# Kernel tuning notes

Hardware: AMD Instinct MI355X
Metric: run time of the kernel (lower is better)

The kernel has to match this reference:

```python
import jax, jax.numpy as jnp
import numpy as np

N = 100000          # nodes
E = 1600000         # edges
DIMS = [128, 64, 64, 47]  # in_feats -> hidden -> hidden -> n_classes
EPS = 1e-5


def setup_inputs() -> dict:
    key = jax.random.key(0)
    ks = jax.random.split(key, 10)
    d = {
        "features": jax.random.normal(ks[0], (N, DIMS[0]), jnp.float32),
        "src": jax.random.randint(ks[1], (E,), 0, N, dtype=jnp.int64),
        "dst": jax.random.randint(ks[2], (E,), 0, N, dtype=jnp.int64),
    }
    # GraphConv weights (glorot-ish) + bias
    for i in range(3):
        fan_in, fan_out = DIMS[i], DIMS[i + 1]
        scale = jnp.sqrt(2.0 / (fan_in + fan_out)).astype(jnp.float32)
        d[f"W{i}"] = jax.random.normal(ks[3 + i], (fan_in, fan_out), jnp.float32) * scale
        d[f"b{i}"] = jnp.zeros((fan_out,), jnp.float32)
    # BatchNorm affine params for the first two layers
    for i in range(2):
        d[f"gamma{i}"] = jnp.ones((DIMS[i + 1],), jnp.float32)
        d[f"beta{i}"] = jnp.zeros((DIMS[i + 1],), jnp.float32)
    return d


def _degree_isqrt(idx):
    # clamp degree to >=1 like DGL, then D^{-1/2}
    deg = jax.ops.segment_sum(jnp.ones((E,), jnp.float32), idx, num_segments=N)
    return jax.lax.rsqrt(jnp.maximum(deg, 1.0))


def _graph_conv(h, W, b, src, dst, out_isqrt, in_isqrt):
    # DGL GraphConv, norm='both': h' = D_in^{-1/2} A D_out^{-1/2} h W + b
    h = h * out_isqrt[:, None]
    if W.shape[0] > W.shape[1]:  # mult W first when it shrinks features (DGL order)
        h = h @ W
        h = jax.ops.segment_sum(h[src], dst, num_segments=N)
    else:
        h = jax.ops.segment_sum(h[src], dst, num_segments=N)
        h = h @ W
    return h * in_isqrt[:, None] + b


def _batch_norm(h, gamma, beta):
    mu = h.mean(axis=0)
    var = h.var(axis=0)  # biased, as torch BatchNorm uses for normalization
    return gamma * (h - mu) * jax.lax.rsqrt(var + EPS) + beta


def reference(features, src, dst, W0, b0, W1, b1, W2, b2,
              gamma0, beta0, gamma1, beta1):
    out_isqrt = _degree_isqrt(src)
    in_isqrt = _degree_isqrt(dst)
    Ws = [(W0, b0), (W1, b1), (W2, b2)]
    bns = [(gamma0, beta0), (gamma1, beta1)]
    h = features
    for i, (W, b) in enumerate(Ws):
        # dropout (p=0.5) before last layer only -> identity in eval mode
        h = _graph_conv(h, W, b, src, dst, out_isqrt, in_isqrt)
        if i < len(Ws) - 1:
            h = _batch_norm(h, *bns[i])
            h = jax.nn.relu(h)
    return h
```

## Files before the change

kernel.cpp:

```cpp
#include <hip/hip_runtime.h>
#include <hip/hip_bf16.h>
#include <hip/hip_fp16.h>

#define BN_EPS 1e-5f
#define N_MAX 100000
#define CAP 64
#define NB_MAX 391
#define BCAP 8192

typedef __attribute__((ext_vector_type(8))) _Float16 half8;
typedef __attribute__((ext_vector_type(4))) float floatx4;

__device__ __attribute__((aligned(16))) float g_wsf[130 * N_MAX + 16384];
__device__ int   g_wsi[(1 + CAP) * N_MAX + NB_MAX * BCAP + 2 * NB_MAX + 64];
__device__ unsigned char g_wsb[NB_MAX * BCAP];

__global__ __launch_bounds__(256)
void k_bin(const int* __restrict__ src, const int* __restrict__ dst,
           int* __restrict__ gcur, int* __restrict__ scur,
           int* __restrict__ pairs, unsigned char* __restrict__ sbytes,
           int E, int nb) {
    __shared__ int dh[NB_MAX], db[NB_MAX], dc[NB_MAX];
    __shared__ int sh[NB_MAX], sb[NB_MAX], sc[NB_MAX];
    const int tid = threadIdx.x;
    for (int i = tid; i < nb; i += 256) { dh[i] = 0; sh[i] = 0; dc[i] = 0; sc[i] = 0; }
    __syncthreads();
    const int e0 = blockIdx.x * 4096;
    int ss[16], dd[16];
#pragma unroll
    for (int i = 0; i < 16; ++i) {
        int e = e0 + i * 256 + tid;
        if (e < E) {
            ss[i] = src[e]; dd[i] = dst[e];
            atomicAdd(&dh[dd[i] >> 8], 1);
            atomicAdd(&sh[ss[i] >> 8], 1);
        } else ss[i] = -1;
    }
    __syncthreads();
    for (int i = tid; i < nb; i += 256) {
        db[i] = atomicAdd(&gcur[i], dh[i]);
        sb[i] = atomicAdd(&scur[i], sh[i]);
    }
    __syncthreads();
#pragma unroll
    for (int i = 0; i < 16; ++i) {
        if (ss[i] >= 0) {
            int b = dd[i] >> 8;
            int idx = db[b] + atomicAdd(&dc[b], 1);
            if (idx < BCAP) pairs[b * BCAP + idx] = (ss[i] << 8) | (dd[i] & 255);
            int b2 = ss[i] >> 8;
            int i2 = sb[b2] + atomicAdd(&sc[b2], 1);
            if (i2 < BCAP) sbytes[b2 * BCAP + i2] = (unsigned char)(ss[i] & 255);
        }
    }
}

__global__ __launch_bounds__(256)
void k_slab(const int* __restrict__ gcur, const int* __restrict__ pairs,
            int* __restrict__ slab, int* __restrict__ cnt,
            float* __restrict__ isq_d, int n) {
    __shared__ int c[256];
    const int tid = threadIdx.x;
    const int d0 = blockIdx.x * 256;
    c[tid] = 0;
    __syncthreads();
    const int m = min(gcur[blockIdx.x], BCAP);
    const int base = blockIdx.x * BCAP;
    for (int i = tid; i < m; i += 256) {
        int p = pairs[base + i];
        int dl = p & 255;
        int slot = atomicAdd(&c[dl], 1);
        if (slot < CAP) slab[(size_t)(d0 + dl) * CAP + slot] = p >> 8;
    }
    __syncthreads();
    int d = d0 + tid;
    if (d < n) {
        cnt[d] = c[tid];
        isq_d[d] = rsqrtf(fmaxf((float)c[tid], 1.0f));
    }
}

__global__ __launch_bounds__(256)
void k_degs(const int* __restrict__ scur, const unsigned char* __restrict__ sbytes,
            float* __restrict__ isq_s, int n) {
    __shared__ int c[256];
    const int tid = threadIdx.x;
    c[tid] = 0;
    __syncthreads();
    const int m = min(scur[blockIdx.x], BCAP);
    const int base = blockIdx.x * BCAP;
    for (int i = tid; i < m; i += 256) atomicAdd(&c[sbytes[base + i]], 1);
    __syncthreads();
    int s = blockIdx.x * 256 + tid;
    if (s < n) isq_s[s] = rsqrtf(fmaxf((float)c[tid], 1.0f));
}

__device__ void wt_fill(const float* __restrict__ W, __half* __restrict__ Wt,
                        int KIN, int KOUT, int ROWS) {
    for (int i = threadIdx.x; i < ROWS * KIN; i += 256) {
        const int c = i / KIN, k = i - c * KIN;
        Wt[c * KIN + k] = (c < KOUT) ? __float2half_rn(W[k * KOUT + c]) : __float2half_rn(0.0f);
    }
}
__global__ __launch_bounds__(256)
void k_wprep(const float* __restrict__ W0, const float* __restrict__ W1,
             const float* __restrict__ W2, __half* __restrict__ Wt0,
             __half* __restrict__ Wt1, __half* __restrict__ Wt2) {
    if (blockIdx.x == 0)      wt_fill(W0, Wt0, 128, 64, 64);
    else if (blockIdx.x == 1) wt_fill(W1, Wt1, 64, 64, 64);
    else                      wt_fill(W2, Wt2, 64, 47, 48);
}

template<bool SB>
__global__ __launch_bounds__(256)
void k_agg(const int* __restrict__ cnt, const int* __restrict__ slab,
           const __half* __restrict__ in, const float* __restrict__ isq_d,
           const float* __restrict__ bias, __half* __restrict__ out, int n) {
    const int d = (int)((blockIdx.x * 256u + threadIdx.x) >> 6);
    if (d >= n) return;
    const int lane = threadIdx.x & 63;
    const int sub = lane >> 3;
    const int fc = (lane & 7) << 3;
    const int m = min(cnt[d], CAP);
    const int* cs = slab + (size_t)d * CAP;
    float a0 = 0.0f, a1 = 0.0f, a2 = 0.0f, a3 = 0.0f;
    float a4 = 0.0f, a5 = 0.0f, a6 = 0.0f, a7 = 0.0f;
    for (int e = 0; e < m; e += 16) {
#pragma unroll
        for (int u = 0; u < 2; ++u) {
            int j = e + u * 8 + sub;
            if (j < m) {
                int s = cs[j];
                const uint4 v = *(const uint4*)(in + (size_t)s * 64 + fc);
                const float2 f0 = __half22float2(*(const __half2*)&v.x);
                const float2 f1 = __half22float2(*(const __half2*)&v.y);
                const float2 f2 = __half22float2(*(const __half2*)&v.z);
                const float2 f3 = __half22float2(*(const __half2*)&v.w);
                a0 += f0.x; a1 += f0.y; a2 += f1.x; a3 += f1.y;
                a4 += f2.x; a5 += f2.y; a6 += f3.x; a7 += f3.y;
            }
        }
    }
#pragma unroll
    for (int sh = 8; sh <= 32; sh <<= 1) {
        a0 += __shfl_xor(a0, sh); a1 += __shfl_xor(a1, sh);
        a2 += __shfl_xor(a2, sh); a3 += __shfl_xor(a3, sh);
        a4 += __shfl_xor(a4, sh); a5 += __shfl_xor(a5, sh);
        a6 += __shfl_xor(a6, sh); a7 += __shfl_xor(a7, sh);
    }
    if (sub == 0) {
        if (SB) {
            const float sd = isq_d[d];
            const float4 b0 = *(const float4*)(bias + fc);
            const float4 b1 = *(const float4*)(bias + fc + 4);
            a0 = a0 * sd + b0.x; a1 = a1 * sd + b0.y;
            a2 = a2 * sd + b0.z; a3 = a3 * sd + b0.w;
            a4 = a4 * sd + b1.x; a5 = a5 * sd + b1.y;
            a6 = a6 * sd + b1.z; a7 = a7 * sd + b1.w;
        }
        __half2 h01 = __floats2half2_rn(a0, a1);
        __half2 h23 = __floats2half2_rn(a2, a3);
        __half2 h45 = __floats2half2_rn(a4, a5);
        __half2 h67 = __floats2half2_rn(a6, a7);
        uint4 u;
        u.x = *(const unsigned*)&h01; u.y = *(const unsigned*)&h23;
        u.z = *(const unsigned*)&h45; u.w = *(const unsigned*)&h67;
        *(uint4*)(out + (size_t)d * 64 + fc) = u;
    }
}

template<int KIN, int KOUTR, bool HIN, bool HOUT, bool BIAS>
__global__ __launch_bounds__(256)
void k_gemm_mfma(const void* __restrict__ Xv, const float* __restrict__ rowscale,
                 const __half* __restrict__ Wt, const float* __restrict__ bias,
                 void* __restrict__ Cv, int n) {
    constexpr int NK = KIN / 32;
    constexpr int NT = (KOUTR + 15) / 16;
    constexpr int CHUNKS = KIN / 8;
    __shared__ __align__(16) unsigned short Xs[64 * KIN];
    const int tid = threadIdx.x;
    const int row0 = blockIdx.x * 64;

#pragma unroll
    for (int it = 0; it < (64 * CHUNKS) / 256; ++it) {
        const int idx = it * 256 + tid;
        const int row = idx / CHUNKS;
        const int ch = idx & (CHUNKS - 1);
        const int rg = row0 + row;
        uint4 v = {0u, 0u, 0u, 0u};
        if (rg < n) {
            if (HIN) {
                v = *(const uint4*)((const __half*)Xv + (size_t)rg * KIN + ch * 8);
            } else {
                const float* Xf = (const float*)Xv;
                const float4 f0 = *(const float4*)(Xf + (size_t)rg * KIN + ch * 8);
                const float4 f1 = *(const float4*)(Xf + (size_t)rg * KIN + ch * 8 + 4);
                __half2 h01 = __floats2half2_rn(f0.x, f0.y);
                __half2 h23 = __floats2half2_rn(f0.z, f0.w);
                __half2 h45 = __floats2half2_rn(f1.x, f1.y);
                __half2 h67 = __floats2half2_rn(f1.z, f1.w);
                v.x = *(const unsigned*)&h01; v.y = *(const unsigned*)&h23;
                v.z = *(const unsigned*)&h45; v.w = *(const unsigned*)&h67;
            }
        }
        const int sch = ch ^ (row & 7);
        *(uint4*)(&Xs[row * KIN + sch * 8]) = v;
    }

    const int lane = tid & 63;
    const int lc = lane & 15;
    const int lg = lane >> 4;
    half8 bf[NK][NT];
#pragma unroll
    for (int s = 0; s < NK; ++s)
#pragma unroll
        for (int t = 0; t < NT; ++t)
            bf[s][t] = *(const half8*)(Wt + (size_t)(t * 16 + lc) * KIN + s * 32 + lg * 8);

    __syncthreads();

    const int w = tid >> 6;
    const int rowl = 16 * w + lc;
    floatx4 acc[NT];
#pragma unroll
    for (int t = 0; t < NT; ++t) acc[t] = 0.0f;
#pragma unroll
    for (int s = 0; s < NK; ++s) {
        const int ch = s * 4 + lg;
        const int sch = ch ^ (rowl & 7);
        const half8 a = *(const half8*)(&Xs[rowl * KIN + sch * 8]);
#pragma unroll
        for (int t = 0; t < NT; ++t)
            acc[t] = __builtin_amdgcn_mfma_f32_16x16x32_f16(a, bf[s][t], acc[t], 0, 0, 0);
    }

    const int rbase = row0 + 16 * w + lg * 4;
#pragma unroll
    for (int t = 0; t < NT; ++t) {
        const int c = t * 16 + lc;
#pragma unroll
        for (int r = 0; r < 4; ++r) {
            const int rg = rbase + r;
            if (rg >= n) continue;
            float v = acc[t][r] * rowscale[rg];
            if (BIAS) v += bias[c];
            if (HOUT) {
                ((__half*)Cv)[(size_t)rg * KOUTR + c] = __float2half_rn(v);
            } else {
                if (KOUTR == 64 || c < KOUTR)
                    ((float*)Cv)[(size_t)rg * KOUTR + c] = v;
            }
        }
    }
}

template<bool HIN>
__global__ __launch_bounds__(256)
void k_bn_stats(const void* __restrict__ Av, float* __restrict__ stats, int n) {
    const int f = threadIdx.x & 63;
    const int sub = threadIdx.x >> 6;
    float s = 0.0f, q = 0.0f;
    for (int i = blockIdx.x * 4 + sub; i < n; i += gridDim.x * 4) {
        float h;
        if (HIN) h = __half2float(((const __half*)Av)[(size_t)i * 64 + f]);
        else     h = ((const float*)Av)[(size_t)i * 64 + f];
        s += h;
        q += h * h;
    }
    __shared__ float ls[4][64], lq[4][64];
    ls[sub][f] = s; lq[sub][f] = q;
    __syncthreads();
    if (sub == 0) {
        s = ls[0][f] + ls[1][f] + ls[2][f] + ls[3][f];
        q = lq[0][f] + lq[1][f] + lq[2][f] + lq[3][f];
        atomicAdd(&stats[f], s);
        atomicAdd(&stats[64 + f], q);
    }
}

template<bool HIN>
__global__ __launch_bounds__(256)
void k_bn_apply(const void* __restrict__ Av, const float* __restrict__ gamma,
                const float* __restrict__ beta, const float* __restrict__ stats,
                const float* __restrict__ outscale, __half* __restrict__ B, int n) {
    unsigned gid = blockIdx.x * 256u + threadIdx.x;
    unsigned i = gid >> 4;
    if (i >= (unsigned)n) return;
    unsigned fq = (gid & 15u) << 2;
    const float invn = 1.0f / (float)n;
    const float4 sm = *(const float4*)(stats + fq);
    const float4 sq = *(const float4*)(stats + 64 + fq);
    const float4 g  = *(const float4*)(gamma + fq);
    const float4 be = *(const float4*)(beta + fq);
    float4 h;
    if (HIN) {
        const uint2 u = *(const uint2*)((const __half*)Av + (size_t)i * 64 + fq);
        const float2 p0 = __half22float2(*(const __half2*)&u.x);
        const float2 p1 = __half22float2(*(const __half2*)&u.y);
        h.x = p0.x; h.y = p0.y; h.z = p1.x; h.w = p1.y;
    } else {
        h = *(const float4*)((const float*)Av + (size_t)i * 64 + fq);
    }
    const float os = outscale[i];
    float4 r;
    { float mu = sm.x * invn, var = sq.x * invn - mu * mu;
      r.x = fmaxf(g.x * (h.x - mu) * rsqrtf(var + BN_EPS) + be.x, 0.0f) * os; }
    { float mu = sm.y * invn, var = sq.y * invn - mu * mu;
      r.y = fmaxf(g.y * (h.y - mu) * rsqrtf(var + BN_EPS) + be.y, 0.0f) * os; }
    { float mu = sm.z * invn, var = sq.z * invn - mu * mu;
      r.z = fmaxf(g.z * (h.z - mu) * rsqrtf(var + BN_EPS) + be.z, 0.0f) * os; }
    { float mu = sm.w * invn, var = sq.w * invn - mu * mu;
      r.w = fmaxf(g.w * (h.w - mu) * rsqrtf(var + BN_EPS) + be.w, 0.0f) * os; }
    __half2 h01 = __floats2half2_rn(r.x, r.y);
    __half2 h23 = __floats2half2_rn(r.z, r.w);
    uint2 u;
    u.x = *(const unsigned*)&h01;
    u.y = *(const unsigned*)&h23;
    *(uint2*)(B + (size_t)i * 64 + fq) = u;
}

extern "C" void kernel_launch(void* const* d_in, const int* in_sizes, int n_in,
                              void* d_out, int out_size, void* d_ws, size_t ws_size,
                              hipStream_t stream) {
    const float* feat = (const float*)d_in[0];
    const int* src  = (const int*)d_in[1];
    const int* dst  = (const int*)d_in[2];
    const float* W0  = (const float*)d_in[3];
    const float* b0  = (const float*)d_in[4];
    const float* W1  = (const float*)d_in[5];
    const float* b1  = (const float*)d_in[6];
    const float* W2  = (const float*)d_in[7];
    const float* b2  = (const float*)d_in[8];
    const float* g0  = (const float*)d_in[9];
    const float* be0 = (const float*)d_in[10];
    const float* g1  = (const float*)d_in[11];
    const float* be1 = (const float*)d_in[12];

    const int n = out_size / 47;
    const int E = in_sizes[1];
    const int nb = (n + 255) >> 8;

    float* wsf = nullptr; int* wsi = nullptr; unsigned char* wsb = nullptr;
    hipGetSymbolAddress((void**)&wsf, HIP_SYMBOL(g_wsf));
    hipGetSymbolAddress((void**)&wsi, HIP_SYMBOL(g_wsi));
    hipGetSymbolAddress((void**)&wsb, HIP_SYMBOL(g_wsb));
    float* isq_s = wsf;
    float* isq_d = wsf + n;
    float* buf1  = wsf + 2 * (size_t)n;
    float* buf2  = buf1 + (size_t)n * 64;
    float* stats = buf2 + (size_t)n * 64;
    __half* Wt0  = (__half*)(stats + 256);
    __half* Wt1  = Wt0 + 64 * 128;
    __half* Wt2  = Wt1 + 64 * 64;
    __half* buf1h = (__half*)buf1;
    __half* buf2h = (__half*)buf2;
    int* cnt     = wsi;
    int* slab    = wsi + n;
    int* pairs   = wsi + (size_t)(1 + CAP) * n;
    int* gcur    = pairs + (size_t)NB_MAX * BCAP;
    int* scur    = gcur + NB_MAX;

    const int gB = (E + 4095) / 4096;
    const int gW = (n + 3) / 4;
    const int gG = (n + 63) / 64;
    const int gA = (n * 16 + 255) / 256;

    hipMemsetAsync(gcur, 0, 2 * NB_MAX * sizeof(int), stream);
    hipMemsetAsync(stats, 0, 256 * sizeof(float), stream);
    k_wprep<<<3, 256, 0, stream>>>(W0, W1, W2, Wt0, Wt1, Wt2);
    k_bin<<<gB, 256, 0, stream>>>(src, dst, gcur, scur, pairs, wsb, E, nb);
    k_slab<<<nb, 256, 0, stream>>>(gcur, pairs, slab, cnt, isq_d, n);
    k_degs<<<nb, 256, 0, stream>>>(scur, wsb, isq_s, n);

    k_gemm_mfma<128, 64, false, true, false><<<gG, 256, 0, stream>>>(feat, isq_s, Wt0, nullptr, buf1h, n);
    k_agg<true><<<gW, 256, 0, stream>>>(cnt, slab, buf1h, isq_d, b0, buf2h, n);
    k_bn_stats<true><<<512, 256, 0, stream>>>(buf2h, stats, n);
    k_bn_apply<true><<<gA, 256, 0, stream>>>(buf2h, g0, be0, stats, isq_s, buf1h, n);

    k_agg<false><<<gW, 256, 0, stream>>>(cnt, slab, buf1h, nullptr, nullptr, buf2h, n);
    k_gemm_mfma<64, 64, true, false, true><<<gG, 256, 0, stream>>>(buf2h, isq_d, Wt1, b1, buf1, n);
    k_bn_stats<false><<<512, 256, 0, stream>>>(buf1, stats + 128, n);
    k_bn_apply<false><<<gA, 256, 0, stream>>>(buf1, g1, be1, stats + 128, isq_s, buf2h, n);

    k_agg<false><<<gW, 256, 0, stream>>>(cnt, slab, buf2h, nullptr, nullptr, buf1h, n);
    k_gemm_mfma<64, 47, true, false, true><<<gG, 256, 0, stream>>>(buf1h, isq_d, Wt2, b2, (float*)d_out, n);
}
```

Before: 463.4 us.

## Fuse BN-apply into aggregation gather, use global-atomic source degrees, merge setup

BatchNorm+ReLU+out-degree scaling is now applied on the fly inside the neighbor gather, so the two separate bn_apply passes and their intermediate writes are gone. Source degrees are counted with global atomics in k_bin, replacing the byte-binning and k_degs pass. The memsets and weight prep are merged into one setup kernel, and layer 2's GEMM now emits fp16 instead of fp32. The cost is that the BN transform is recomputed once per edge instead of once per node, plus an extra isq_s gather per edge and more contended global atomics.

```diff
diff --git a/kernel.cpp b/kernel.cpp
--- a/kernel.cpp
+++ b/kernel.cpp
@@ -12,18 +12,42 @@
 typedef __attribute__((ext_vector_type(4))) float floatx4;
 
 __device__ __attribute__((aligned(16))) float g_wsf[130 * N_MAX + 16384];
-__device__ int   g_wsi[(1 + CAP) * N_MAX + NB_MAX * BCAP + 2 * NB_MAX + 64];
-__device__ unsigned char g_wsb[NB_MAX * BCAP];
+__device__ int   g_wsi[(2 + CAP) * N_MAX + NB_MAX * BCAP + NB_MAX + 64];
+
+__device__ void wt_fill(const float* __restrict__ W, __half* __restrict__ Wt,
+                        int KIN, int KOUT, int ROWS) {
+    for (int i = threadIdx.x; i < ROWS * KIN; i += 256) {
+        const int c = i / KIN, k = i - c * KIN;
+        Wt[c * KIN + k] = (c < KOUT) ? __float2half_rn(W[k * KOUT + c]) : __float2half_rn(0.0f);
+    }
+}
+__global__ __launch_bounds__(256)
+void k_setup(const float* __restrict__ W0, const float* __restrict__ W1,
+             const float* __restrict__ W2, __half* __restrict__ Wt0,
+             __half* __restrict__ Wt1, __half* __restrict__ Wt2,
+             int* __restrict__ degs, int* __restrict__ gcur,
+             float* __restrict__ stats, int n, int nb) {
+    const int b = blockIdx.x;
+    if (b == 0)      wt_fill(W0, Wt0, 128, 64, 64);
+    else if (b == 1) wt_fill(W1, Wt1, 64, 64, 64);
+    else if (b == 2) wt_fill(W2, Wt2, 64, 47, 48);
+    else {
+        for (int i = (b - 3) * 256 + threadIdx.x; i < n; i += (gridDim.x - 3) * 256)
+            degs[i] = 0;
+        if (b == 3) {
+            for (int i = threadIdx.x; i < nb; i += 256) gcur[i] = 0;
+            stats[threadIdx.x] = 0.0f;
+        }
+    }
+}
 
 __global__ __launch_bounds__(256)
 void k_bin(const int* __restrict__ src, const int* __restrict__ dst,
-           int* __restrict__ gcur, int* __restrict__ scur,
-           int* __restrict__ pairs, unsigned char* __restrict__ sbytes,
-           int E, int nb) {
+           int* __restrict__ gcur, int* __restrict__ degs,
+           int* __restrict__ pairs, int E, int nb) {
     __shared__ int dh[NB_MAX], db[NB_MAX], dc[NB_MAX];
-    __shared__ int sh[NB_MAX], sb[NB_MAX], sc[NB_MAX];
     const int tid = threadIdx.x;
-    for (int i = tid; i < nb; i += 256) { dh[i] = 0; sh[i] = 0; dc[i] = 0; sc[i] = 0; }
+    for (int i = tid; i < nb; i += 256) { dh[i] = 0; dc[i] = 0; }
     __syncthreads();
     const int e0 = blockIdx.x * 4096;
     int ss[16], dd[16];
@@ -33,14 +57,11 @@
         if (e < E) {
             ss[i] = src[e]; dd[i] = dst[e];
             atomicAdd(&dh[dd[i] >> 8], 1);
-            atomicAdd(&sh[ss[i] >> 8], 1);
+            atomicAdd(&degs[ss[i]], 1);
         } else ss[i] = -1;
     }
     __syncthreads();
-    for (int i = tid; i < nb; i += 256) {
-        db[i] = atomicAdd(&gcur[i], dh[i]);
-        sb[i] = atomicAdd(&scur[i], sh[i]);
-    }
+    for (int i = tid; i < nb; i += 256) db[i] = atomicAdd(&gcur[i], dh[i]);
     __syncthreads();
 #pragma unroll
     for (int i = 0; i < 16; ++i) {
@@ -48,17 +69,15 @@
             int b = dd[i] >> 8;
             int idx = db[b] + atomicAdd(&dc[b], 1);
             if (idx < BCAP) pairs[b * BCAP + idx] = (ss[i] << 8) | (dd[i] & 255);
-            int b2 = ss[i] >> 8;
-            int i2 = sb[b2] + atomicAdd(&sc[b2], 1);
-            if (i2 < BCAP) sbytes[b2 * BCAP + i2] = (unsigned char)(ss[i] & 255);
         }
     }
 }
 
 __global__ __launch_bounds__(256)
 void k_slab(const int* __restrict__ gcur, const int* __restrict__ pairs,
-            int* __restrict__ slab, int* __restrict__ cnt,
-            float* __restrict__ isq_d, int n) {
+            const int* __restrict__ degs, int* __restrict__ slab,
+            int* __restrict__ cnt, float* __restrict__ isq_d,
+            float* __restrict__ isq_s, int n) {
     __shared__ int c[256];
     const int tid = threadIdx.x;
     const int d0 = blockIdx.x * 256;
@@ -77,91 +96,83 @@
     if (d < n) {
         cnt[d] = c[tid];
         isq_d[d] = rsqrtf(fmaxf((float)c[tid], 1.0f));
-    }
-}
-
-__global__ __launch_bounds__(256)
-void k_degs(const int* __restrict__ scur, const unsigned char* __restrict__ sbytes,
-            float* __restrict__ isq_s, int n) {
-    __shared__ int c[256];
-    const int tid = threadIdx.x;
-    c[tid] = 0;
-    __syncthreads();
-    const int m = min(scur[blockIdx.x], BCAP);
-    const int base = blockIdx.x * BCAP;
-    for (int i = tid; i < m; i += 256) atomicAdd(&c[sbytes[base + i]], 1);
-    __syncthreads();
-    int s = blockIdx.x * 256 + tid;
-    if (s < n) isq_s[s] = rsqrtf(fmaxf((float)c[tid], 1.0f));
-}
-
-__device__ void wt_fill(const float* __restrict__ W, __half* __restrict__ Wt,
-                        int KIN, int KOUT, int ROWS) {
-    for (int i = threadIdx.x; i < ROWS * KIN; i += 256) {
-        const int c = i / KIN, k = i - c * KIN;
-        Wt[c * KIN + k] = (c < KOUT) ? __float2half_rn(W[k * KOUT + c]) : __float2half_rn(0.0f);
-    }
-}
-__global__ __launch_bounds__(256)
-void k_wprep(const float* __restrict__ W0, const float* __restrict__ W1,
-             const float* __restrict__ W2, __half* __restrict__ Wt0,
-             __half* __restrict__ Wt1, __half* __restrict__ Wt2) {
-    if (blockIdx.x == 0)      wt_fill(W0, Wt0, 128, 64, 64);
-    else if (blockIdx.x == 1) wt_fill(W1, Wt1, 64, 64, 64);
-    else                      wt_fill(W2, Wt2, 64, 47, 48);
-}
-
-template<bool SB>
+        isq_s[d] = rsqrtf(fmaxf((float)degs[d], 1.0f));
+    }
+}
+
+template<bool SB, bool FBN>
 __global__ __launch_bounds__(256)
 void k_agg(const int* __restrict__ cnt, const int* __restrict__ slab,
            const __half* __restrict__ in, const float* __restrict__ isq_d,
-           const float* __restrict__ bias, __half* __restrict__ out, int n) {
+           const float* __restrict__ bias, const float* __restrict__ stats,
+           const float* __restrict__ gamma, const float* __restrict__ beta,
+           const float* __restrict__ isq_s, __half* __restrict__ out, int n) {
     const int d = (int)((blockIdx.x * 256u + threadIdx.x) >> 6);
     if (d >= n) return;
     const int lane = threadIdx.x & 63;
     const int sub = lane >> 3;
     const int fc = (lane & 7) << 3;
+
+    float bsc[8], bsh[8];
+    if (FBN) {
+        const float invn = 1.0f / (float)n;
+#pragma unroll
+        for (int k = 0; k < 8; ++k) {
+            const int f = fc + k;
+            const float mu = stats[f] * invn;
+            const float var = stats[64 + f] * invn - mu * mu;
+            const float s = gamma[f] * rsqrtf(var + BN_EPS);
+            bsc[k] = s;
+            bsh[k] = beta[f] - mu * s;
+        }
+    }
+
     const int m = min(cnt[d], CAP);
     const int* cs = slab + (size_t)d * CAP;
-    float a0 = 0.0f, a1 = 0.0f, a2 = 0.0f, a3 = 0.0f;
-    float a4 = 0.0f, a5 = 0.0f, a6 = 0.0f, a7 = 0.0f;
+    float a[8] = {};
     for (int e = 0; e < m; e += 16) {
 #pragma unroll
         for (int u = 0; u < 2; ++u) {
             int j = e + u * 8 + sub;
             if (j < m) {
                 int s = cs[j];
+                float iss;
+                if (FBN) iss = isq_s[s];
                 const uint4 v = *(const uint4*)(in + (size_t)s * 64 + fc);
                 const float2 f0 = __half22float2(*(const __half2*)&v.x);
                 const float2 f1 = __half22float2(*(const __half2*)&v.y);
                 const float2 f2 = __half22float2(*(const __half2*)&v.z);
                 const float2 f3 = __half22float2(*(const __half2*)&v.w);
-                a0 += f0.x; a1 += f0.y; a2 += f1.x; a3 += f1.y;
-                a4 += f2.x; a5 += f2.y; a6 += f3.x; a7 += f3.y;
+                float h[8] = {f0.x, f0.y, f1.x, f1.y, f2.x, f2.y, f3.x, f3.y};
+                if (FBN) {
+#pragma unroll
+                    for (int k = 0; k < 8; ++k)
+                        h[k] = fmaxf(fmaf(h[k], bsc[k], bsh[k]), 0.0f) * iss;
+                }
+#pragma unroll
+                for (int k = 0; k < 8; ++k) a[k] += h[k];
             }
         }
     }
 #pragma unroll
     for (int sh = 8; sh <= 32; sh <<= 1) {
-        a0 += __shfl_xor(a0, sh); a1 += __shfl_xor(a1, sh);
-        a2 += __shfl_xor(a2, sh); a3 += __shfl_xor(a3, sh);
-        a4 += __shfl_xor(a4, sh); a5 += __shfl_xor(a5, sh);
-        a6 += __shfl_xor(a6, sh); a7 += __shfl_xor(a7, sh);
+#pragma unroll
+        for (int k = 0; k < 8; ++k) a[k] += __shfl_xor(a[k], sh);
     }
     if (sub == 0) {
         if (SB) {
             const float sd = isq_d[d];
             const float4 b0 = *(const float4*)(bias + fc);
             const float4 b1 = *(const float4*)(bias + fc + 4);
-            a0 = a0 * sd + b0.x; a1 = a1 * sd + b0.y;
-            a2 = a2 * sd + b0.z; a3 = a3 * sd + b0.w;
-            a4 = a4 * sd + b1.x; a5 = a5 * sd + b1.y;
-            a6 = a6 * sd + b1.z; a7 = a7 * sd + b1.w;
-        }
-        __half2 h01 = __floats2half2_rn(a0, a1);
-        __half2 h23 = __floats2half2_rn(a2, a3);
-        __half2 h45 = __floats2half2_rn(a4, a5);
-        __half2 h67 = __floats2half2_rn(a6, a7);
+            a[0] = a[0] * sd + b0.x; a[1] = a[1] * sd + b0.y;
+            a[2] = a[2] * sd + b0.z; a[3] = a[3] * sd + b0.w;
+            a[4] = a[4] * sd + b1.x; a[5] = a[5] * sd + b1.y;
+            a[6] = a[6] * sd + b1.z; a[7] = a[7] * sd + b1.w;
+        }
+        __half2 h01 = __floats2half2_rn(a[0], a[1]);
+        __half2 h23 = __floats2half2_rn(a[2], a[3]);
+        __half2 h45 = __floats2half2_rn(a[4], a[5]);
+        __half2 h67 = __floats2half2_rn(a[6], a[7]);
         uint4 u;
         u.x = *(const unsigned*)&h01; u.y = *(const unsigned*)&h23;
         u.z = *(const unsigned*)&h45; u.w = *(const unsigned*)&h67;
@@ -278,47 +289,6 @@
     }
 }
 
-template<bool HIN>
-__global__ __launch_bounds__(256)
-void k_bn_apply(const void* __restrict__ Av, const float* __restrict__ gamma,
-                const float* __restrict__ beta, const float* __restrict__ stats,
-                const float* __restrict__ outscale, __half* __restrict__ B, int n) {
-    unsigned gid = blockIdx.x * 256u + threadIdx.x;
-    unsigned i = gid >> 4;
-    if (i >= (unsigned)n) return;
-    unsigned fq = (gid & 15u) << 2;
-    const float invn = 1.0f / (float)n;
-    const float4 sm = *(const float4*)(stats + fq);
-    const float4 sq = *(const float4*)(stats + 64 + fq);
-    const float4 g  = *(const float4*)(gamma + fq);
-    const float4 be = *(const float4*)(beta + fq);
-    float4 h;
-    if (HIN) {
-        const uint2 u = *(const uint2*)((const __half*)Av + (size_t)i * 64 + fq);
-        const float2 p0 = __half22float2(*(const __half2*)&u.x);
-        const float2 p1 = __half22float2(*(const __half2*)&u.y);
-        h.x = p0.x; h.y = p0.y; h.z = p1.x; h.w = p1.y;
-    } else {
-        h = *(const float4*)((const float*)Av + (size_t)i * 64 + fq);
-    }
-    const float os = outscale[i];
-    float4 r;
-    { float mu = sm.x * invn, var = sq.x * invn - mu * mu;
-      r.x = fmaxf(g.x * (h.x - mu) * rsqrtf(var + BN_EPS) + be.x, 0.0f) * os; }
-    { float mu = sm.y * invn, var = sq.y * invn - mu * mu;
-      r.y = fmaxf(g.y * (h.y - mu) * rsqrtf(var + BN_EPS) + be.y, 0.0f) * os; }
-    { float mu = sm.z * invn, var = sq.z * invn - mu * mu;
-      r.z = fmaxf(g.z * (h.z - mu) * rsqrtf(var + BN_EPS) + be.z, 0.0f) * os; }
-    { float mu = sm.w * invn, var = sq.w * invn - mu * mu;
-      r.w = fmaxf(g.w * (h.w - mu) * rsqrtf(var + BN_EPS) + be.w, 0.0f) * os; }
-    __half2 h01 = __floats2half2_rn(r.x, r.y);
-    __half2 h23 = __floats2half2_rn(r.z, r.w);
-    uint2 u;
-    u.x = *(const unsigned*)&h01;
-    u.y = *(const unsigned*)&h23;
-    *(uint2*)(B + (size_t)i * 64 + fq) = u;
-}
-
 extern "C" void kernel_launch(void* const* d_in, const int* in_sizes, int n_in,
                               void* d_out, int out_size, void* d_ws, size_t ws_size,
                               hipStream_t stream) {
@@ -340,10 +310,9 @@
     const int E = in_sizes[1];
     const int nb = (n + 255) >> 8;
 
-    float* wsf = nullptr; int* wsi = nullptr; unsigned char* wsb = nullptr;
+    float* wsf = nullptr; int* wsi = nullptr;
     hipGetSymbolAddress((void**)&wsf, HIP_SYMBOL(g_wsf));
     hipGetSymbolAddress((void**)&wsi, HIP_SYMBOL(g_wsi));
-    hipGetSymbolAddress((void**)&wsb, HIP_SYMBOL(g_wsb));
     float* isq_s = wsf;
     float* isq_d = wsf + n;
     float* buf1  = wsf + 2 * (size_t)n;
@@ -355,33 +324,30 @@
     __half* buf1h = (__half*)buf1;
     __half* buf2h = (__half*)buf2;
     int* cnt     = wsi;
-    int* slab    = wsi + n;
-    int* pairs   = wsi + (size_t)(1 + CAP) * n;
+    int* degs    = wsi + n;
+    int* slab    = wsi + 2 * (size_t)n;
+    int* pairs   = slab + (size_t)N_MAX * CAP;
     int* gcur    = pairs + (size_t)NB_MAX * BCAP;
-    int* scur    = gcur + NB_MAX;
 
     const int gB = (E + 4095) / 4096;
     const int gW = (n + 3) / 4;
     const int gG = (n + 63) / 64;
-    const int gA = (n * 16 + 255) / 256;
-
-    hipMemsetAsync(gcur, 0, 2 * NB_MAX * sizeof(int), stream);
-    hipMemsetAsync(stats, 0, 256 * sizeof(float), stream);
-    k_wprep<<<3, 256, 0, stream>>>(W0, W1, W2, Wt0, Wt1, Wt2);
-    k_bin<<<gB, 256, 0, stream>>>(src, dst, gcur, scur, pairs, wsb, E, nb);
-    k_slab<<<nb, 256, 0, stream>>>(gcur, pairs, slab, cnt, isq_d, n);
-    k_degs<<<nb, 256, 0, stream>>>(scur, wsb, isq_s, n);
+
+    k_setup<<<35, 256, 0, stream>>>(W0, W1, W2, Wt0, Wt1, Wt2, degs, gcur, stats, n, nb);
+    k_bin<<<gB, 256, 0, stream>>>(src, dst, gcur, degs, pairs, E, nb);
+    k_slab<<<nb, 256, 0, stream>>>(gcur, pairs, degs, slab, cnt, isq_d, isq_s, n);
 
     k_gemm_mfma<128, 64, false, true, false><<<gG, 256, 0, stream>>>(feat, isq_s, Wt0, nullptr, buf1h, n);
-    k_agg<true><<<gW, 256, 0, stream>>>(cnt, slab, buf1h, isq_d, b0, buf2h, n);
+    k_agg<true, false><<<gW, 256, 0, stream>>>(cnt, slab, buf1h, isq_d, b0,
+                                               nullptr, nullptr, nullptr, nullptr, buf2h, n);
     k_bn_stats<true><<<512, 256, 0, stream>>>(buf2h, stats, n);
-    k_bn_apply<true><<<gA, 256, 0, stream>>>(buf2h, g0, be0, stats, isq_s, buf1h, n);
-
-    k_agg<false><<<gW, 256, 0, stream>>>(cnt, slab, buf1h, nullptr, nullptr, buf2h, n);
-    k_gemm_mfma<64, 64, true, false, true><<<gG, 256, 0, stream>>>(buf2h, isq_d, Wt1, b1, buf1, n);
-    k_bn_stats<false><<<512, 256, 0, stream>>>(buf1, stats + 128, n);
-    k_bn_apply<false><<<gA, 256, 0, stream>>>(buf1, g1, be1, stats + 128, isq_s, buf2h, n);
-
-    k_agg<false><<<gW, 256, 0, stream>>>(cnt, slab, buf2h, nullptr, nullptr, buf1h, n);
+
+    k_agg<false, true><<<gW, 256, 0, stream>>>(cnt, slab, buf2h, nullptr, nullptr,
+                                               stats, g0, be0, isq_s, buf1h, n);
+    k_gemm_mfma<64, 64, true, true, true><<<gG, 256, 0, stream>>>(buf1h, isq_d, Wt1, b1, buf2h, n);
+    k_bn_stats<true><<<512, 256, 0, stream>>>(buf2h, stats + 128, n);
+
+    k_agg<false, true><<<gW, 256, 0, stream>>>(cnt, slab, buf2h, nullptr, nullptr,
+                                               stats + 128, g1, be1, isq_s, buf1h, n);
     k_gemm_mfma<64, 47, true, false, true><<<gG, 256, 0, stream>>>(buf1h, isq_d, Wt2, b2, (float*)d_out, n);
 }
```

New measurement: 492.2 us. +6.2%, slower.
